# Performance work log

Hardware: AMD Instinct MI355X
Metric: run time of the kernel (lower is better)

The kernel has to match this reference:

```python
import jax, jax.numpy as jnp
import numpy as np

MARGIN = 1.0
N, D = 8192, 256
NUM_CLASSES = 32


def setup_inputs() -> dict:
    key = jax.random.key(0)
    k1, k2 = jax.random.split(key)
    embeddings = jax.random.normal(k1, (N, D), dtype=jnp.float32)
    labels = jax.random.randint(k2, (N,), 0, NUM_CLASSES, dtype=jnp.int64)
    return {"embeddings": embeddings, "labels": labels}


def reference(embeddings, labels):
    # L2-normalize rows (F.normalize p=2 dim=1); subsequent cosine similarity
    # of unit vectors is just their dot product -> plain [N, N] matmul.
    e = embeddings / jnp.linalg.norm(embeddings, axis=1, keepdims=True)
    sim = e @ e.T  # [N, N] cosine similarity matrix

    pos_mask = (labels[:, None] == labels[None, :])  # [N, N] bool
    pos_count = jnp.sum(pos_mask)
    neg_count = pos_mask.size - pos_count

    # Fused masked-mean reductions (no boolean gather / dynamic shapes).
    pos_term = jnp.where(pos_mask, (1.0 - sim) ** 2, 0.0)
    neg_term = jnp.where(pos_mask, 0.0, jax.nn.relu(sim - MARGIN) ** 2)
    positive_loss = jnp.sum(pos_term) / pos_count
    negative_loss = jnp.sum(neg_term) / neg_count
    return positive_loss + negative_loss
```

## Files before the change

### kernel.cpp

```cpp
#include <hip/hip_runtime.h>
#include <hip/hip_bf16.h>
#include <stdint.h>

#define N_ROWS 8192
#define DIM 256
#define NUM_CLASSES 32
#define PC 384
#define TPC 6
#define NBLK3 (NUM_CLASSES * TPC)

typedef __attribute__((ext_vector_type(4))) float f32x4;
typedef __attribute__((ext_vector_type(8))) short bf16x8;

static __device__ inline unsigned short f2bf(float f) {
  union { float f; unsigned u; } v; v.f = f;
  unsigned r = v.u + 0x7FFFu + ((v.u >> 16) & 1u);
  return (unsigned short)(r >> 16);
}

static __device__ inline void async_copy16(const void* g, void* l) {
  __builtin_amdgcn_global_load_lds(
      (const __attribute__((address_space(1))) unsigned int*)g,
      (__attribute__((address_space(3))) unsigned int*)l, 16, 0, 0);
}

__global__ __launch_bounds__(256)
void normalize_kernel(const float* __restrict__ emb, unsigned short* __restrict__ en) {
  const int row = blockIdx.x * 4 + (threadIdx.x >> 6);
  const int lane = threadIdx.x & 63;
  const float4 v = reinterpret_cast<const float4*>(emb + (size_t)row * DIM)[lane];
  float s = v.x * v.x + v.y * v.y + v.z * v.z + v.w * v.w;
  #pragma unroll
  for (int o = 32; o; o >>= 1) s += __shfl_xor(s, o);
  const float inv = 1.0f / sqrtf(s);
  ushort4 o4;
  o4.x = f2bf(v.x * inv);
  o4.y = f2bf(v.y * inv);
  o4.z = f2bf(v.z * inv);
  o4.w = f2bf(v.w * inv);
  reinterpret_cast<ushort4*>(en + (size_t)row * DIM)[lane] = o4;
}

__global__ __launch_bounds__(1024)
void prep_kernel(const int* __restrict__ labels,
                 unsigned short* __restrict__ en,
                 unsigned short* __restrict__ rowlist,
                 int* __restrict__ cnt) {
  __shared__ int h[NUM_CLASSES], rk[NUM_CLASSES];
  const int t = threadIdx.x;
  if (t < NUM_CLASSES) { h[t] = 0; rk[t] = 0; }
  __syncthreads();
  for (int i = t; i < N_ROWS; i += 1024) atomicAdd(&h[labels[i]], 1);
  for (int i = t; i < NUM_CLASSES * PC / 2; i += 1024)
    ((int*)rowlist)[i] = 0x20002000;
  if (t < 128) ((int*)(en + (size_t)N_ROWS * DIM))[t] = 0;
  __syncthreads();
  if (t < NUM_CLASSES) cnt[t] = h[t];
  for (int i = t; i < N_ROWS; i += 1024) {
    const int c = labels[i];
    const int r = atomicAdd(&rk[c], 1);
    if (r < PC) rowlist[c * PC + r] = (unsigned short)i;
  }
}

__global__ __launch_bounds__(256)
void class_sim_kernel(const unsigned short* __restrict__ en,
                      const unsigned short* __restrict__ rowlist,
                      const int* __restrict__ cnt,
                      float2* __restrict__ parts) {
  const int b = blockIdx.x;
  const int c = b / TPC, q = b - c * TPC;
  const int ti = (q < 3) ? 0 : (q < 5) ? 1 : 2;
  const int tj = (q < 3) ? q : (q < 5) ? (q - 2) : 2;
  const int t = threadIdx.x;
  const int nc = cnt[c];
  if (ti * 128 >= nc || tj * 128 >= nc) {
    if (t == 0) parts[b] = (float2){0.f, 0.f};
    return;
  }

  __shared__ __align__(16) short lA[2][128 * 64];
  __shared__ __align__(16) short lB[2][128 * 64];
  __shared__ float red[8];

  const int lane = t & 63;
  const int wid = t >> 6;
  const int r15 = lane & 15;
  const int wm = (wid >> 1) * 64;
  const int wn = (wid & 1) * 64;

  int rA[4], rB[4];
  #pragma unroll
  for (int it = 0; it < 4; ++it) {
    rA[it] = rowlist[c * PC + ti * 128 + it * 32 + (t >> 3)];
    rB[it] = rowlist[c * PC + tj * 128 + it * 32 + (t >> 3)];
  }
  const int cb = (((t & 7) ^ ((t >> 3) & 7)) << 4);

  auto stage = [&](int buf, int kt) {
    const int kb = kt * 128;
    #pragma unroll
    for (int it = 0; it < 4; ++it) {
      const int x = (it * 256 + t) * 16;
      async_copy16((const char*)en + (size_t)rA[it] * 512 + kb + cb,
                   (char*)&lA[buf][0] + x);
      async_copy16((const char*)en + (size_t)rB[it] * 512 + kb + cb,
                   (char*)&lB[buf][0] + x);
    }
  };

  f32x4 accf[4][4];
  #pragma unroll
  for (int i = 0; i < 4; ++i)
    #pragma unroll
    for (int j = 0; j < 4; ++j) accf[i][j] = (f32x4){0.f, 0.f, 0.f, 0.f};

  stage(0, 0);
  __syncthreads();

  int cur = 0;
  #pragma unroll
  for (int kt = 0; kt < 4; ++kt) {
    if (kt < 3) stage(cur ^ 1, kt + 1);

    #pragma unroll
    for (int kk = 0; kk < 2; ++kk) {
      const int cbase = kk * 64 + ((lane >> 4) << 4);
      bf16x8 af[4], bf[4];
      #pragma unroll
      for (int mi = 0; mi < 4; ++mi) {
        const int row = wm + mi * 16 + r15;
        const int off = row * 128 + (cbase ^ ((row & 7) << 4));
        af[mi] = *(const bf16x8*)((const char*)&lA[cur][0] + off);
      }
      #pragma unroll
      for (int ni = 0; ni < 4; ++ni) {
        const int row = wn + ni * 16 + r15;
        const int off = row * 128 + (cbase ^ ((row & 7) << 4));
        bf[ni] = *(const bf16x8*)((const char*)&lB[cur][0] + off);
      }
      #pragma unroll
      for (int mi = 0; mi < 4; ++mi)
        #pragma unroll
        for (int ni = 0; ni < 4; ++ni)
          accf[mi][ni] = __builtin_amdgcn_mfma_f32_16x16x32_bf16(
              af[mi], bf[ni], accf[mi][ni], 0, 0, 0);
    }

    if (kt < 3) { __syncthreads(); cur ^= 1; }
  }

  float s1 = 0.f, s2 = 0.f;
  #pragma unroll
  for (int mi = 0; mi < 4; ++mi)
    #pragma unroll
    for (int ni = 0; ni < 4; ++ni)
      #pragma unroll
      for (int j = 0; j < 4; ++j) {
        const float s = accf[mi][ni][j];
        s1 += s;
        s2 += s * s;
      }
  if (ti != tj) { s1 *= 2.f; s2 *= 2.f; }

  #pragma unroll
  for (int o = 32; o; o >>= 1) { s1 += __shfl_down(s1, o); s2 += __shfl_down(s2, o); }
  if (lane == 0) { red[wid * 2] = s1; red[wid * 2 + 1] = s2; }
  __syncthreads();
  if (t == 0) {
    float2 v;
    v.x = red[0] + red[2] + red[4] + red[6];
    v.y = red[1] + red[3] + red[5] + red[7];
    parts[b] = v;
  }
}

__global__ __launch_bounds__(64)
void finalize_kernel(const int* __restrict__ cnt,
                     const float2* __restrict__ parts,
                     float* __restrict__ out) {
  const int t = threadIdx.x;
  float s1 = 0.f, s2 = 0.f;
  for (int i = t; i < NBLK3; i += 64) { float2 v = parts[i]; s1 += v.x; s2 += v.y; }
  #pragma unroll
  for (int o = 32; o; o >>= 1) { s1 += __shfl_down(s1, o); s2 += __shfl_down(s2, o); }
  if (t == 0) {
    float P = 0.f;
    for (int c = 0; c < NUM_CLASSES; ++c) { const float n = (float)cnt[c]; P += n * n; }
    out[0] = (P - 2.f * s1 + s2) / P;
  }
}

extern "C" void kernel_launch(void* const* d_in, const int* in_sizes, int n_in,
                              void* d_out, int out_size, void* d_ws, size_t ws_size,
                              hipStream_t stream) {
  const float* emb = (const float*)d_in[0];
  const int* labels = (const int*)d_in[1];
  float* out = (float*)d_out;

  unsigned short* en = (unsigned short*)d_ws;
  char* p = (char*)d_ws + (size_t)(N_ROWS + 1) * DIM * 2;
  unsigned short* rowlist = (unsigned short*)p;
  p += NUM_CLASSES * PC * 2;
  int* cnt = (int*)p;
  p += NUM_CLASSES * 4;
  float2* parts = (float2*)p;

  normalize_kernel<<<N_ROWS / 4, 256, 0, stream>>>(emb, en);
  prep_kernel<<<1, 1024, 0, stream>>>(labels, en, rowlist, cnt);
  class_sim_kernel<<<NBLK3, 256, 0, stream>>>(en, rowlist, cnt, parts);
  finalize_kernel<<<1, 64, 0, stream>>>(cnt, parts, out);
}
```

Baseline: 24.14 us.

## Merge normalize and prep kernels; fold finalize into sim kernel via atomics

Normalization and label bucketing now run in one launch, with a single extra block of 256 threads doing the prep work. The finalize kernel is removed: each sim block atomically adds its partial sums, and the last block to arrive (found through an atomic counter) computes the output. This cuts four launches down to two, saving launch and inter-kernel gap overhead. In exchange, prep runs serially in one 256-thread block alongside the normalize blocks, float atomics make the sum order nondeterministic, and there is a global counter handoff.

```diff
diff --git a/kernel.cpp b/kernel.cpp
--- a/kernel.cpp
+++ b/kernel.cpp
@@ -25,38 +25,47 @@
 }
 
 __global__ __launch_bounds__(256)
-void normalize_kernel(const float* __restrict__ emb, unsigned short* __restrict__ en) {
-  const int row = blockIdx.x * 4 + (threadIdx.x >> 6);
-  const int lane = threadIdx.x & 63;
-  const float4 v = reinterpret_cast<const float4*>(emb + (size_t)row * DIM)[lane];
-  float s = v.x * v.x + v.y * v.y + v.z * v.z + v.w * v.w;
-  #pragma unroll
-  for (int o = 32; o; o >>= 1) s += __shfl_xor(s, o);
-  const float inv = 1.0f / sqrtf(s);
-  ushort4 o4;
-  o4.x = f2bf(v.x * inv);
-  o4.y = f2bf(v.y * inv);
-  o4.z = f2bf(v.z * inv);
-  o4.w = f2bf(v.w * inv);
-  reinterpret_cast<ushort4*>(en + (size_t)row * DIM)[lane] = o4;
-}
-
-__global__ __launch_bounds__(1024)
-void prep_kernel(const int* __restrict__ labels,
-                 unsigned short* __restrict__ en,
-                 unsigned short* __restrict__ rowlist,
-                 int* __restrict__ cnt) {
+void norm_prep_kernel(const float* __restrict__ emb,
+                      const int* __restrict__ labels,
+                      unsigned short* __restrict__ en,
+                      unsigned short* __restrict__ rowlist,
+                      int* __restrict__ cnt,
+                      float* __restrict__ acc,
+                      int* __restrict__ counter) {
+  const int t = threadIdx.x;
+  if (blockIdx.x < 2048) {
+    const int row = blockIdx.x * 4 + (t >> 6);
+    const int lane = t & 63;
+    const float4 v = reinterpret_cast<const float4*>(emb + (size_t)row * DIM)[lane];
+    float s = v.x * v.x + v.y * v.y + v.z * v.z + v.w * v.w;
+    #pragma unroll
+    for (int o = 32; o; o >>= 1) s += __shfl_xor(s, o);
+    const float inv = 1.0f / sqrtf(s);
+    ushort4 o4;
+    o4.x = f2bf(v.x * inv);
+    o4.y = f2bf(v.y * inv);
+    o4.z = f2bf(v.z * inv);
+    o4.w = f2bf(v.w * inv);
+    reinterpret_cast<ushort4*>(en + (size_t)row * DIM)[lane] = o4;
+    return;
+  }
+
   __shared__ int h[NUM_CLASSES], rk[NUM_CLASSES];
-  const int t = threadIdx.x;
   if (t < NUM_CLASSES) { h[t] = 0; rk[t] = 0; }
   __syncthreads();
-  for (int i = t; i < N_ROWS; i += 1024) atomicAdd(&h[labels[i]], 1);
-  for (int i = t; i < NUM_CLASSES * PC / 2; i += 1024)
+  for (int i = t; i < N_ROWS; i += 256) atomicAdd(&h[labels[i]], 1);
+  for (int i = t; i < NUM_CLASSES * PC / 2; i += 256)
     ((int*)rowlist)[i] = 0x20002000;
   if (t < 128) ((int*)(en + (size_t)N_ROWS * DIM))[t] = 0;
+  if (t == 0) { acc[0] = 0.f; acc[1] = 0.f; counter[0] = 0; }
   __syncthreads();
   if (t < NUM_CLASSES) cnt[t] = h[t];
-  for (int i = t; i < N_ROWS; i += 1024) {
+  if (t == 0) {
+    float P = 0.f;
+    for (int c = 0; c < NUM_CLASSES; ++c) { const float n = (float)h[c]; P += n * n; }
+    acc[2] = P;
+  }
+  for (int i = t; i < N_ROWS; i += 256) {
     const int c = labels[i];
     const int r = atomicAdd(&rk[c], 1);
     if (r < PC) rowlist[c * PC + r] = (unsigned short)i;
@@ -67,127 +76,127 @@
 void class_sim_kernel(const unsigned short* __restrict__ en,
                       const unsigned short* __restrict__ rowlist,
                       const int* __restrict__ cnt,
-                      float2* __restrict__ parts) {
+                      float* __restrict__ acc,
+                      int* __restrict__ counter,
+                      float* __restrict__ out) {
   const int b = blockIdx.x;
   const int c = b / TPC, q = b - c * TPC;
   const int ti = (q < 3) ? 0 : (q < 5) ? 1 : 2;
   const int tj = (q < 3) ? q : (q < 5) ? (q - 2) : 2;
   const int t = threadIdx.x;
   const int nc = cnt[c];
-  if (ti * 128 >= nc || tj * 128 >= nc) {
-    if (t == 0) parts[b] = (float2){0.f, 0.f};
-    return;
-  }
-
-  __shared__ __align__(16) short lA[2][128 * 64];
-  __shared__ __align__(16) short lB[2][128 * 64];
-  __shared__ float red[8];
-
-  const int lane = t & 63;
-  const int wid = t >> 6;
-  const int r15 = lane & 15;
-  const int wm = (wid >> 1) * 64;
-  const int wn = (wid & 1) * 64;
-
-  int rA[4], rB[4];
-  #pragma unroll
-  for (int it = 0; it < 4; ++it) {
-    rA[it] = rowlist[c * PC + ti * 128 + it * 32 + (t >> 3)];
-    rB[it] = rowlist[c * PC + tj * 128 + it * 32 + (t >> 3)];
-  }
-  const int cb = (((t & 7) ^ ((t >> 3) & 7)) << 4);
-
-  auto stage = [&](int buf, int kt) {
-    const int kb = kt * 128;
+  const bool active = (ti * 128 < nc) && (tj * 128 < nc);
+
+  float s1 = 0.f, s2 = 0.f;
+
+  if (active) {
+    __shared__ __align__(16) short lA[2][128 * 64];
+    __shared__ __align__(16) short lB[2][128 * 64];
+    __shared__ float red[8];
+
+    const int lane = t & 63;
+    const int wid = t >> 6;
+    const int r15 = lane & 15;
+    const int wm = (wid >> 1) * 64;
+    const int wn = (wid & 1) * 64;
+
+    int rA[4], rB[4];
     #pragma unroll
     for (int it = 0; it < 4; ++it) {
-      const int x = (it * 256 + t) * 16;
-      async_copy16((const char*)en + (size_t)rA[it] * 512 + kb + cb,
-                   (char*)&lA[buf][0] + x);
-      async_copy16((const char*)en + (size_t)rB[it] * 512 + kb + cb,
-                   (char*)&lB[buf][0] + x);
-    }
-  };
-
-  f32x4 accf[4][4];
-  #pragma unroll
-  for (int i = 0; i < 4; ++i)
-    #pragma unroll
-    for (int j = 0; j < 4; ++j) accf[i][j] = (f32x4){0.f, 0.f, 0.f, 0.f};
-
-  stage(0, 0);
-  __syncthreads();
-
-  int cur = 0;
-  #pragma unroll
-  for (int kt = 0; kt < 4; ++kt) {
-    if (kt < 3) stage(cur ^ 1, kt + 1);
-
-    #pragma unroll
-    for (int kk = 0; kk < 2; ++kk) {
-      const int cbase = kk * 64 + ((lane >> 4) << 4);
-      bf16x8 af[4], bf[4];
-      #pragma unroll
-      for (int mi = 0; mi < 4; ++mi) {
-        const int row = wm + mi * 16 + r15;
-        const int off = row * 128 + (cbase ^ ((row & 7) << 4));
-        af[mi] = *(const bf16x8*)((const char*)&lA[cur][0] + off);
+      rA[it] = rowlist[c * PC + ti * 128 + it * 32 + (t >> 3)];
+      rB[it] = rowlist[c * PC + tj * 128 + it * 32 + (t >> 3)];
+    }
+    const int cb = (((t & 7) ^ ((t >> 3) & 7)) << 4);
+
+    auto stage = [&](int buf, int kt) {
+      const int kb = kt * 128;
+      #pragma unroll
+      for (int it = 0; it < 4; ++it) {
+        const int x = (it * 256 + t) * 16;
+        async_copy16((const char*)en + (size_t)rA[it] * 512 + kb + cb,
+                     (char*)&lA[buf][0] + x);
+        async_copy16((const char*)en + (size_t)rB[it] * 512 + kb + cb,
+                     (char*)&lB[buf][0] + x);
       }
-      #pragma unroll
-      for (int ni = 0; ni < 4; ++ni) {
-        const int row = wn + ni * 16 + r15;
-        const int off = row * 128 + (cbase ^ ((row & 7) << 4));
-        bf[ni] = *(const bf16x8*)((const char*)&lB[cur][0] + off);
+    };
+
+    f32x4 accf[4][4];
+    #pragma unroll
+    for (int i = 0; i < 4; ++i)
+      #pragma unroll
+      for (int j = 0; j < 4; ++j) accf[i][j] = (f32x4){0.f, 0.f, 0.f, 0.f};
+
+    stage(0, 0);
+    __syncthreads();
+
+    int cur = 0;
+    #pragma unroll
+    for (int kt = 0; kt < 4; ++kt) {
+      if (kt < 3) stage(cur ^ 1, kt + 1);
+
+      #pragma unroll
+      for (int kk = 0; kk < 2; ++kk) {
+        const int cbase = kk * 64 + ((lane >> 4) << 4);
+        bf16x8 af[4], bf[4];
+        #pragma unroll
+        for (int mi = 0; mi < 4; ++mi) {
+          const int row = wm + mi * 16 + r15;
+          const int off = row * 128 + (cbase ^ ((row & 7) << 4));
+          af[mi] = *(const bf16x8*)((const char*)&lA[cur][0] + off);
+        }
+        #pragma unroll
+        for (int ni = 0; ni < 4; ++ni) {
+          const int row = wn + ni * 16 + r15;
+          const int off = row * 128 + (cbase ^ ((row & 7) << 4));
+          bf[ni] = *(const bf16x8*)((const char*)&lB[cur][0] + off);
+        }
+        #pragma unroll
+        for (int mi = 0; mi < 4; ++mi)
+          #pragma unroll
+          for (int ni = 0; ni < 4; ++ni)
+            accf[mi][ni] = __builtin_amdgcn_mfma_f32_16x16x32_bf16(
+                af[mi], bf[ni], accf[mi][ni], 0, 0, 0);
       }
-      #pragma unroll
-      for (int mi = 0; mi < 4; ++mi)
-        #pragma unroll
-        for (int ni = 0; ni < 4; ++ni)
-          accf[mi][ni] = __builtin_amdgcn_mfma_f32_16x16x32_bf16(
-              af[mi], bf[ni], accf[mi][ni], 0, 0, 0);
-    }
-
-    if (kt < 3) { __syncthreads(); cur ^= 1; }
-  }
-
-  float s1 = 0.f, s2 = 0.f;
-  #pragma unroll
-  for (int mi = 0; mi < 4; ++mi)
-    #pragma unroll
-    for (int ni = 0; ni < 4; ++ni)
-      #pragma unroll
-      for (int j = 0; j < 4; ++j) {
-        const float s = accf[mi][ni][j];
-        s1 += s;
-        s2 += s * s;
-      }
-  if (ti != tj) { s1 *= 2.f; s2 *= 2.f; }
-
-  #pragma unroll
-  for (int o = 32; o; o >>= 1) { s1 += __shfl_down(s1, o); s2 += __shfl_down(s2, o); }
-  if (lane == 0) { red[wid * 2] = s1; red[wid * 2 + 1] = s2; }
-  __syncthreads();
+
+      if (kt < 3) { __syncthreads(); cur ^= 1; }
+    }
+
+    #pragma unroll
+    for (int mi = 0; mi < 4; ++mi)
+      #pragma unroll
+      for (int ni = 0; ni < 4; ++ni)
+        #pragma unroll
+        for (int j = 0; j < 4; ++j) {
+          const float s = accf[mi][ni][j];
+          s1 += s;
+          s2 += s * s;
+        }
+    if (ti != tj) { s1 *= 2.f; s2 *= 2.f; }
+
+    #pragma unroll
+    for (int o = 32; o; o >>= 1) { s1 += __shfl_down(s1, o); s2 += __shfl_down(s2, o); }
+    if (lane == 0) { red[wid * 2] = s1; red[wid * 2 + 1] = s2; }
+    __syncthreads();
+    if (t == 0) {
+      s1 = red[0] + red[2] + red[4] + red[6];
+      s2 = red[1] + red[3] + red[5] + red[7];
+    }
+  }
+
   if (t == 0) {
-    float2 v;
-    v.x = red[0] + red[2] + red[4] + red[6];
-    v.y = red[1] + red[3] + red[5] + red[7];
-    parts[b] = v;
-  }
-}
-
-__global__ __launch_bounds__(64)
-void finalize_kernel(const int* __restrict__ cnt,
-                     const float2* __restrict__ parts,
-                     float* __restrict__ out) {
-  const int t = threadIdx.x;
-  float s1 = 0.f, s2 = 0.f;
-  for (int i = t; i < NBLK3; i += 64) { float2 v = parts[i]; s1 += v.x; s2 += v.y; }
-  #pragma unroll
-  for (int o = 32; o; o >>= 1) { s1 += __shfl_down(s1, o); s2 += __shfl_down(s2, o); }
-  if (t == 0) {
-    float P = 0.f;
-    for (int c = 0; c < NUM_CLASSES; ++c) { const float n = (float)cnt[c]; P += n * n; }
-    out[0] = (P - 2.f * s1 + s2) / P;
+    if (active) {
+      atomicAdd(&acc[0], s1);
+      atomicAdd(&acc[1], s2);
+    }
+    __threadfence();
+    const int prev = atomicAdd(counter, 1);
+    if (prev == NBLK3 - 1) {
+      __threadfence();
+      const float ts1 = atomicAdd(&acc[0], 0.f);
+      const float ts2 = atomicAdd(&acc[1], 0.f);
+      const float P = acc[2];
+      out[0] = (P - 2.f * ts1 + ts2) / P;
+    }
   }
 }
 
@@ -204,10 +213,10 @@
   p += NUM_CLASSES * PC * 2;
   int* cnt = (int*)p;
   p += NUM_CLASSES * 4;
-  float2* parts = (float2*)p;
-
-  normalize_kernel<<<N_ROWS / 4, 256, 0, stream>>>(emb, en);
-  prep_kernel<<<1, 1024, 0, stream>>>(labels, en, rowlist, cnt);
-  class_sim_kernel<<<NBLK3, 256, 0, stream>>>(en, rowlist, cnt, parts);
-  finalize_kernel<<<1, 64, 0, stream>>>(cnt, parts, out);
-}
+  float* acc = (float*)p;
+  p += 4 * 4;
+  int* counter = (int*)p;
+
+  norm_prep_kernel<<<2049, 256, 0, stream>>>(emb, labels, en, rowlist, cnt, acc, counter);
+  class_sim_kernel<<<NBLK3, 256, 0, stream>>>(en, rowlist, cnt, acc, counter, out);
+}
```

Result: slower. 31.94 us (+32.3%).
